# Performance work log

Hardware: AMD Instinct MI355X
Metric: run time of the kernel (lower is better)

## Reference

```python
import jax, jax.numpy as jnp
import numpy as np

N_SRC = 16384   # src nodes in block (includes dst nodes first, per DGL convention)
N_DST = 8192    # dst nodes
K = 32          # fixed in-degree per dst node -> dense mailbox [N_DST, K]
E = N_DST * K   # 262144 edges; edge i has dst node i // K
T = 16          # padded edge-sequence length
NODE_IN = 64
H = 64          # node_hidden_dim
E_IN = 8        # edge_in_dim
TH = 8          # time_hidden_dim
D_IN = E_IN + TH


def lstm_last(x, lengths, Wih, Whh, bih, bhh):
    """Unidirectional 1-layer LSTM; returns hidden state at step lengths-1 (pack_padded h_n).
    x: (E, T, D); lengths: (E,) in [1, T]. PyTorch gate order: i, f, g, o."""
    n, t_max, _ = x.shape
    h0 = jnp.zeros((n, H), x.dtype)

    def step(carry, xt):
        h, c, hlast, t = carry
        g = xt @ Wih.T + bih + h @ Whh.T + bhh
        i, f, gg, o = jnp.split(g, 4, axis=-1)
        c = jax.nn.sigmoid(f) * c + jax.nn.sigmoid(i) * jnp.tanh(gg)
        h = jax.nn.sigmoid(o) * jnp.tanh(c)
        hlast = jnp.where((t < lengths)[:, None], h, hlast)
        return (h, c, hlast, t + 1), None

    init = (h0, h0, h0, jnp.int32(0))
    (_, _, hlast, _), _ = jax.lax.scan(step, init, jnp.swapaxes(x, 0, 1))
    return hlast  # (E, H)


def sparsemax(z):
    """Sparsemax over last axis (Martins & Astudillo), matching the torch code."""
    z = z - jnp.max(z, axis=-1, keepdims=True)
    zs = -jnp.sort(-z, axis=-1)  # descending
    r = jnp.arange(1, z.shape[-1] + 1, dtype=z.dtype)
    bound = 1.0 + r * zs
    cs = jnp.cumsum(zs, axis=-1)
    is_gt = (bound > cs).astype(z.dtype)
    k = jnp.max(is_gt * r, axis=-1, keepdims=True)
    taus = (jnp.sum(is_gt * zs, axis=-1, keepdims=True) - 1.0) / k
    return jnp.maximum(z - taus, 0.0)


def setup_inputs():
    key = jax.random.key(0)
    ks = jax.random.split(key, 24)
    s = 0.1
    inp = {}
    inp["node_features"] = jax.random.normal(ks[0], (N_SRC, NODE_IN), jnp.float32)
    inp["edge_feats"] = jax.random.normal(ks[1], (E, T, E_IN), jnp.float32)
    inp["e_times"] = jax.random.uniform(ks[2], (E, T), jnp.float32)
    inp["e_len"] = jax.random.randint(ks[3], (E,), 1, T + 1).astype(jnp.int32)
    inp["edge_src"] = jax.random.randint(ks[4], (E,), 0, N_SRC).astype(jnp.int32)
    # Time2Vec (SineActivation) params: v = cat([sin(tau@w + b), tau@w0 + b0])
    inp["t2v_w"] = s * jax.random.normal(ks[5], (1, TH - 1), jnp.float32)
    inp["t2v_b"] = s * jax.random.normal(ks[6], (1, TH - 1), jnp.float32)
    inp["t2v_w0"] = s * jax.random.normal(ks[7], (1, 1), jnp.float32)
    inp["t2v_b0"] = s * jax.random.normal(ks[8], (1, 1), jnp.float32)
    # edge_layer LSTM
    inp["lstm_e_Wih"] = s * jax.random.normal(ks[9], (4 * H, D_IN), jnp.float32)
    inp["lstm_e_Whh"] = s * jax.random.normal(ks[10], (4 * H, H), jnp.float32)
    inp["lstm_e_bih"] = s * jax.random.normal(ks[11], (4 * H,), jnp.float32)
    inp["lstm_e_bhh"] = s * jax.random.normal(ks[12], (4 * H,), jnp.float32)
    # edge_attn_layer LSTM
    inp["lstm_a_Wih"] = s * jax.random.normal(ks[13], (4 * H, D_IN), jnp.float32)
    inp["lstm_a_Whh"] = s * jax.random.normal(ks[14], (4 * H, H), jnp.float32)
    inp["lstm_a_bih"] = s * jax.random.normal(ks[15], (4 * H,), jnp.float32)
    inp["lstm_a_bhh"] = s * jax.random.normal(ks[16], (4 * H,), jnp.float32)
    # attention scorer (no bias), edge_out and node linears
    inp["attn_w"] = s * jax.random.normal(ks[17], (H, 1), jnp.float32)
    inp["edge_out_W"] = s * jax.random.normal(ks[18], (H, NODE_IN + H), jnp.float32)
    inp["edge_out_b"] = s * jax.random.normal(ks[19], (H,), jnp.float32)
    inp["node_W"] = s * jax.random.normal(ks[20], (H, NODE_IN + H), jnp.float32)
    inp["node_b"] = s * jax.random.normal(ks[21], (H,), jnp.float32)
    return inp


def reference(node_features, edge_feats, e_times, t2v_w, t2v_b, t2v_w0, t2v_b0,
              lstm_e_Wih, lstm_e_Whh, lstm_e_bih, lstm_e_bhh,
              lstm_a_Wih, lstm_a_Whh, lstm_a_bih, lstm_a_bhh,
              attn_w, edge_out_W, edge_out_b, node_W, node_b,
              e_len, edge_src):
    h_src = node_features                 # dropout is identity in eval
    h_dst = node_features[:N_DST]
    # Time2Vec: tau (E, T, 1) -> (E, T, TH)
    tau = e_times[..., None]
    tenc = jnp.concatenate([jnp.sin(tau * t2v_w[0] + t2v_b[0]),
                            tau * t2v_w0[0] + t2v_b0[0]], axis=-1)
    e = jnp.concatenate([edge_feats, tenc], axis=-1)  # (E, T, D_IN)
    # per-edge LSTM encodings (last valid step)
    e_out = lstm_last(e, e_len, lstm_e_Wih, lstm_e_Whh, lstm_e_bih, lstm_e_bhh)  # (E, H)
    a_out = lstm_last(e, e_len, lstm_a_Wih, lstm_a_Whh, lstm_a_bih, lstm_a_bhh)  # (E, H)
    a = jax.nn.leaky_relu(a_out @ attn_w, 0.01)  # (E, 1)
    # per-edge message
    m = jax.nn.relu(jnp.concatenate([h_src[edge_src], e_out], axis=-1) @ edge_out_W.T + edge_out_b)  # (E, H)
    # reduce over ragged mailbox (regular degree K -> dense [N_DST, K, H])
    mb = m.reshape(N_DST, K, H)
    alpha = sparsemax(a.reshape(N_DST, K))[..., None]  # (N_DST, K, 1)
    h_neigh = jnp.sum(alpha * mb, axis=1)              # (N_DST, H)
    h = jax.nn.relu(jnp.concatenate([h_dst, h_neigh], axis=-1) @ node_W.T + node_b)
    return h  # (N_DST, H)
```

## Files before the change

kernel.cpp:

```cpp
#include <hip/hip_runtime.h>

typedef __bf16 bf16;
typedef __bf16 bf16x8 __attribute__((ext_vector_type(8)));
typedef float f32x4 __attribute__((ext_vector_type(4)));

#define N_DSTN 8192
#define TT 16
#define HROW 72
#define HBUF (32 * HROW)

#define WS_WHH  0
#define WS_WIH  65536
#define WS_BIAS 81920
#define WS_EW   83968
#define WS_NW   100352
#define WS_EB   116736
#define WS_NB   116992
#define WS_ATTN 117248
#define WS_T2W  117504
#define WS_T2B  117536

__device__ __forceinline__ f32x4 MFMA(bf16x8 a, bf16x8 b, f32x4 c) {
    return __builtin_amdgcn_mfma_f32_16x16x32_bf16(a, b, c, 0, 0, 0);
}
__device__ __forceinline__ float ldf(const void* p, long i, bool isb) {
    return isb ? (float)((const bf16*)p)[i] : ((const float*)p)[i];
}
__device__ __forceinline__ bf16x8 zero8() {
    bf16x8 z;
    #pragma unroll
    for (int i = 0; i < 8; i++) z[i] = (bf16)0.0f;
    return z;
}
__device__ __forceinline__ bf16x8 ld8v(const void* p, long i, bool isb) {
    if (isb) {
        return *reinterpret_cast<const bf16x8*>((const bf16*)p + i);
    } else {
        const float* f = (const float*)p + i;
        float4 u = *reinterpret_cast<const float4*>(f);
        float4 v = *reinterpret_cast<const float4*>(f + 4);
        bf16x8 r;
        r[0] = (bf16)u.x; r[1] = (bf16)u.y; r[2] = (bf16)u.z; r[3] = (bf16)u.w;
        r[4] = (bf16)v.x; r[5] = (bf16)v.y; r[6] = (bf16)v.z; r[7] = (bf16)v.w;
        return r;
    }
}

extern "C" __global__ void gtea_prep(const void* __restrict__ e_times,
                                     const void* __restrict__ t2v_w,
                                     const void* __restrict__ t2v_b,
                                     const void* __restrict__ t2v_w0,
                                     const void* __restrict__ t2v_b0,
                                     const void* __restrict__ Wih_e,
                                     const void* __restrict__ Whh_e,
                                     const void* __restrict__ bih_e,
                                     const void* __restrict__ bhh_e,
                                     const void* __restrict__ Wih_a,
                                     const void* __restrict__ Whh_a,
                                     const void* __restrict__ bih_a,
                                     const void* __restrict__ bhh_a,
                                     const void* __restrict__ attn_w,
                                     const void* __restrict__ edge_out_W,
                                     const void* __restrict__ edge_out_b,
                                     const void* __restrict__ node_W,
                                     const void* __restrict__ node_b,
                                     void* __restrict__ ws)
{
    __shared__ int isb_s;
    const int tid = threadIdx.x;
    if (tid < 64) {
        const unsigned short* u = (const unsigned short*)e_times;
        unsigned short a = u[tid * 2], b = u[tid * 2 + 1];
        bool ok = (a <= 0x3F80u) && (b <= 0x3F80u);
        unsigned long long m = __ballot(ok);
        if (tid == 0) isb_s = (m == ~0ULL) ? 1 : 0;
    }
    __syncthreads();
    const bool isb = (isb_s != 0);
    char* wsb = (char*)ws;
    const int gstep = blockDim.x * gridDim.x;
    const int g0 = blockIdx.x * blockDim.x + tid;

    for (int i = g0; i < 2 * 256 * 64; i += gstep) {
        int Lw = i >> 14, rem = i & 16383, n = rem >> 6;
        const void* W = Lw ? Whh_a : Whh_e;
        float gs = ((n >> 6) == 2) ? 2.88539008f : -1.44269504f;
        ((bf16*)(wsb + WS_WHH))[i] = (bf16)(ldf(W, rem, isb) * gs);
    }
    for (int i = g0; i < 2 * 256 * 16; i += gstep) {
        int Lw = i >> 12, rem = i & 4095, n = rem >> 4;
        const void* W = Lw ? Wih_a : Wih_e;
        float gs = ((n >> 6) == 2) ? 2.88539008f : -1.44269504f;
        ((bf16*)(wsb + WS_WIH))[i] = (bf16)(ldf(W, rem, isb) * gs);
    }
    for (int i = g0; i < 2 * 256; i += gstep) {
        int Lw = i >> 8, n = i & 255;
        const void* bi = Lw ? bih_a : bih_e;
        const void* bh = Lw ? bhh_a : bhh_e;
        float gs = ((n >> 6) == 2) ? 2.88539008f : -1.44269504f;
        ((float*)(wsb + WS_BIAS))[i] = (ldf(bi, n, isb) + ldf(bh, n, isb)) * gs;
    }
    for (int i = g0; i < 64 * 128; i += gstep) {
        ((bf16*)(wsb + WS_EW))[i] = (bf16)ldf(edge_out_W, i, isb);
        ((bf16*)(wsb + WS_NW))[i] = (bf16)ldf(node_W, i, isb);
    }
    for (int i = g0; i < 64; i += gstep) {
        ((float*)(wsb + WS_EB))[i]   = ldf(edge_out_b, i, isb);
        ((float*)(wsb + WS_NB))[i]   = ldf(node_b, i, isb);
        ((float*)(wsb + WS_ATTN))[i] = ldf(attn_w, i, isb);
    }
    if (g0 < 7) {
        ((float*)(wsb + WS_T2W))[g0] = ldf(t2v_w, g0, isb);
        ((float*)(wsb + WS_T2B))[g0] = ldf(t2v_b, g0, isb);
    }
    if (g0 == 7) {
        ((float*)(wsb + WS_T2W))[7] = ldf(t2v_w0, 0, isb);
        ((float*)(wsb + WS_T2B))[7] = ldf(t2v_b0, 0, isb);
    }
}

extern "C" __global__ void __launch_bounds__(512, 4)
gtea_fused(const void* __restrict__ node_features,
           const void* __restrict__ edge_feats,
           const void* __restrict__ e_times,
           const int*  __restrict__ e_len,
           const int*  __restrict__ edge_src,
           const void* __restrict__ ws,
           void* __restrict__ outp)
{
    __shared__ __align__(16) bf16 habuf[2][2][HBUF];
    __shared__ __align__(16) bf16 featb[TT * 32 * 8];
    __shared__ __align__(16) bf16 tb[TT * 32 * 8];
    __shared__ float t2w[8], t2b[8];
    __shared__ float attn_f[64];
    __shared__ float vbuf[128];
    __shared__ float scores_sh[32], alpha_sh[32];
    __shared__ int   lens_sh[32], idx_sh[32];
    __shared__ int   isb_sh;

    const int tid = threadIdx.x;
    const int w   = tid >> 6;
    const int l   = tid & 63;
    const int l15 = l & 15;
    const int q   = l >> 4;
    const int L   = w >> 2;
    const int w4  = w & 3;
    const int u16 = w4 * 16 + l15;

    const int d  = blockIdx.x;
    const int e0 = d * 32;
    const char* wsb = (const char*)ws;

    if (tid < 64) {
        const unsigned short* u = (const unsigned short*)e_times;
        unsigned short a = u[tid * 2], b = u[tid * 2 + 1];
        bool ok = (a <= 0x3F80u) && (b <= 0x3F80u);
        unsigned long long m = __ballot(ok);
        if (tid == 0) isb_sh = (m == ~0ULL) ? 1 : 0;
    }
    if (tid < 32) {
        int lj = e_len[e0 + tid];
        int rank = 0;
        for (int i = 0; i < 32; i++) {
            int li = __shfl(lj, i);
            rank += (li > lj) || (li == lj && i < tid);
        }
        int mt = rank >> 4, kp = rank & 15;
        int slot = mt * 16 + (kp & 3) * 4 + (kp >> 2);
        idx_sh[slot]  = tid;
        lens_sh[slot] = lj;
    }
    __syncthreads();
    const bool isb = (isb_sh != 0);

    if (tid < 8)  { t2w[tid] = ((const float*)(wsb + WS_T2W))[tid];
                    t2b[tid] = ((const float*)(wsb + WS_T2B))[tid]; }
    if (tid < 64) attn_f[tid] = ((const float*)(wsb + WS_ATTN))[tid];
    if (tid < 64) vbuf[tid] = ldf(node_features, (long)d * 64 + tid, isb);
    {
        unsigned int* hz = reinterpret_cast<unsigned int*>(&habuf[0][0][0]);
        for (int i = tid; i < HBUF / 2; i += 512) { hz[i] = 0u; hz[i + HBUF] = 0u; }
    }
    __syncthreads();

    int gm0[4], gm1[4];
    #pragma unroll
    for (int r = 0; r < 4; r++) {
        gm0[r] = __builtin_amdgcn_readfirstlane(lens_sh[r]);
        gm1[r] = __builtin_amdgcn_readfirstlane(lens_sh[16 + r]);
    }
    const int tmax = gm0[0], mtmax1 = gm1[0];

    unsigned lp = 0;
    #pragma unroll
    for (int mt = 0; mt < 2; mt++)
        #pragma unroll
        for (int r = 0; r < 4; r++)
            lp |= (unsigned)(lens_sh[mt * 16 + q * 4 + r] - 1) << ((mt * 4 + r) * 4);

    {
        int s = tid >> 4, t = tid & 15;
        int j = idx_sh[s];
        long base = ((long)(e0 + j) * TT + t) * 8;
        *reinterpret_cast<bf16x8*>(&featb[(t * 32 + s) * 8]) = ld8v(edge_feats, base, isb);
        float tau = ldf(e_times, (long)(e0 + j) * TT + t, isb);
        bf16x8 te;
        #pragma unroll
        for (int i = 0; i < 7; i++) te[i] = (bf16)__sinf(tau * t2w[i] + t2b[i]);
        te[7] = (bf16)(tau * t2w[7] + t2b[7]);
        *reinterpret_cast<bf16x8*>(&tb[(t * 32 + s) * 8]) = te;
    }

    const bf16*  wWhh  = (const bf16*)(wsb + WS_WHH) + (long)L * 256 * 64;
    const bf16*  wWih  = (const bf16*)(wsb + WS_WIH) + (long)L * 256 * 16;
    const float* wBias = (const float*)(wsb + WS_BIAS) + L * 256;
    bf16x8 Bh[4][2], Bx[4];
    float  bias[4];
    #pragma unroll
    for (int j = 0; j < 4; j++) {
        int n = 64 * j + u16;
        Bh[j][0] = *reinterpret_cast<const bf16x8*>(wWhh + (long)n * 64 + q * 8);
        Bh[j][1] = *reinterpret_cast<const bf16x8*>(wWhh + (long)n * 64 + 32 + q * 8);
        Bx[j] = (q < 2) ? *reinterpret_cast<const bf16x8*>(wWih + (long)n * 16 + q * 8) : zero8();
        bias[j] = wBias[n];
    }

    float c[2][4];
    #pragma unroll
    for (int mt = 0; mt < 2; mt++)
        #pragma unroll
        for (int r = 0; r < 4; r++) c[mt][r] = 0.0f;

    __syncthreads();

    bf16* hb_base = &habuf[L][0][0];
    const int rd_off = l15 * HROW + q * 8;
    const int wr_off = (q * 4) * HROW + u16;

    for (int t = 0; t < tmax; t++) {
        const bf16* hbR = hb_base + (t & 1) * HBUF;
        bf16*       hbW = hb_base + ((t + 1) & 1) * HBUF;

        auto do_mt = [&](int mt) {
            const bf16* hr = hbR + mt * (16 * HROW) + rd_off;
            bf16x8 ah0 = *reinterpret_cast<const bf16x8*>(hr);
            bf16x8 ah1 = *reinterpret_cast<const bf16x8*>(hr + 32);
            bf16x8 xa;
            if (q < 2) {
                const bf16* xp = (q == 0 ? featb : tb) + (t * 32 + mt * 16 + l15) * 8;
                xa = *reinterpret_cast<const bf16x8*>(xp);
            } else {
                xa = zero8();
            }
            f32x4 D[4];
            #pragma unroll
            for (int j = 0; j < 4; j++) {
                f32x4 acc = {bias[j], bias[j], bias[j], bias[j]};
                acc = MFMA(ah0, Bh[j][0], acc);
                acc = MFMA(ah1, Bh[j][1], acc);
                acc = MFMA(xa,  Bx[j],    acc);
                D[j] = acc;
            }
            bf16* hw = hbW + mt * (16 * HROW) + wr_off;
            #pragma unroll
            for (int r = 0; r < 4; r++) {
                int gmax = mt ? gm1[r] : gm0[r];
                if (t < gmax) {
                    int lm1 = (int)((lp >> ((mt * 4 + r) * 4)) & 15u);
                    if (t <= lm1) {
                        float gi = D[0][r], gf = D[1][r];
                        float gg = D[2][r], go = D[3][r];
                        float ei = __builtin_amdgcn_exp2f(gi);
                        float ef = __builtin_amdgcn_exp2f(gf);
                        float eg = __builtin_amdgcn_exp2f(gg);
                        float di = 1.0f + ei, dfv = 1.0f + ef, dg = 1.0f + eg;
                        float m1 = di * dg;
                        float R1 = __builtin_amdgcn_rcpf(m1 * dfv);
                        float cn = (m1 * R1) * c[mt][r] + (eg - 1.0f) * (dfv * R1);
                        c[mt][r] = cn;
                        float eo = __builtin_amdgcn_exp2f(go);
                        float ec = __builtin_amdgcn_exp2f(2.88539008f * cn);
                        float R2 = __builtin_amdgcn_rcpf((1.0f + eo) * (1.0f + ec));
                        float hn = (ec - 1.0f) * R2;
                        hw[r * HROW] = (bf16)hn;
                    }
                }
            }
        };
        do_mt(0);
        if (t < mtmax1) do_mt(1);
        __syncthreads();
    }

    if (tid < 256) {
        int s = tid >> 3, c8 = tid & 7;
        const bf16* ha = &habuf[1][lens_sh[s] & 1][s * HROW];
        float p = 0.0f;
        #pragma unroll
        for (int i = 0; i < 8; i++)
            p += (float)ha[c8 * 8 + i] * attn_f[c8 * 8 + i];
        p += __shfl_xor(p, 1);
        p += __shfl_xor(p, 2);
        p += __shfl_xor(p, 4);
        if (c8 == 0) scores_sh[s] = (p > 0.0f) ? p : 0.01f * p;
    }
    float mval[2][4];
    if (tid < 256) {
        const bf16* wEW = (const bf16*)(wsb + WS_EW);
        bf16x8 Bw[4];
        #pragma unroll
        for (int ks = 0; ks < 4; ks++)
            Bw[ks] = *reinterpret_cast<const bf16x8*>(wEW + (long)u16 * 128 + ks * 32 + q * 8);
        float mb = ((const float*)(wsb + WS_EB))[u16];
        #pragma unroll
        for (int mt = 0; mt < 2; mt++) {
            int s = mt * 16 + l15;
            int src = edge_src[e0 + idx_sh[s]];
            bf16x8 a0 = ld8v(node_features, (long)src * 64 + q * 8, isb);
            bf16x8 a1 = ld8v(node_features, (long)src * 64 + 32 + q * 8, isb);
            const bf16* he = &habuf[0][lens_sh[s] & 1][s * HROW];
            bf16x8 a2 = *reinterpret_cast<const bf16x8*>(he + q * 8);
            bf16x8 a3 = *reinterpret_cast<const bf16x8*>(he + 32 + q * 8);
            f32x4 acc = {mb, mb, mb, mb};
            acc = MFMA(a0, Bw[0], acc);
            acc = MFMA(a1, Bw[1], acc);
            acc = MFMA(a2, Bw[2], acc);
            acc = MFMA(a3, Bw[3], acc);
            #pragma unroll
            for (int r = 0; r < 4; r++) mval[mt][r] = fmaxf(acc[r], 0.0f);
        }
    }
    __syncthreads();

    if (tid < 64) {
        float z = (tid < 32) ? scores_sh[tid] : -3.0e38f;
        float zm = z;
        #pragma unroll
        for (int m = 32; m >= 1; m >>= 1) zm = fmaxf(zm, __shfl_xor(zm, m));
        z -= zm;
        int cnt = 0; float sb = 0.0f;
        for (int i = 0; i < 32; i++) {
            float zi = __shfl(z, i);
            bool before = (zi > z) || (zi == z && i < tid);
            if (before) { cnt++; sb += zi; }
        }
        float r = (float)(cnt + 1);
        float S = sb + z;
        bool isgt = (tid < 32) && (1.0f + r * z > S);
        float kf  = isgt ? r : 0.0f;
        float sgt = isgt ? z : 0.0f;
        #pragma unroll
        for (int m = 32; m >= 1; m >>= 1) kf = fmaxf(kf, __shfl_xor(kf, m));
        #pragma unroll
        for (int m = 32; m >= 1; m >>= 1) sgt += __shfl_xor(sgt, m);
        float tau = (sgt - 1.0f) / fmaxf(kf, 1.0f);
        if (tid < 32) alpha_sh[tid] = fmaxf(z - tau, 0.0f);
    }
    __syncthreads();

    if (tid < 256) {
        float hn = 0.0f;
        #pragma unroll
        for (int mt = 0; mt < 2; mt++)
            #pragma unroll
            for (int r = 0; r < 4; r++)
                hn += alpha_sh[mt * 16 + q * 4 + r] * mval[mt][r];
        hn += __shfl_xor(hn, 16);
        hn += __shfl_xor(hn, 32);
        if (q == 0) vbuf[64 + u16] = hn;
    }
    __syncthreads();

    if (tid < 256) {
        int u = tid >> 2, kq = tid & 3;
        const bf16* wNW = (const bf16*)(wsb + WS_NW);
        bf16x8 wv0 = *reinterpret_cast<const bf16x8*>(wNW + (long)u * 128 + kq * 32);
        bf16x8 wv1 = *reinterpret_cast<const bf16x8*>(wNW + (long)u * 128 + kq * 32 + 8);
        bf16x8 wv2 = *reinterpret_cast<const bf16x8*>(wNW + (long)u * 128 + kq * 32 + 16);
        bf16x8 wv3 = *reinterpret_cast<const bf16x8*>(wNW + (long)u * 128 + kq * 32 + 24);
        float acc = 0.0f;
        #pragma unroll
        for (int i = 0; i < 8; i++) {
            acc += (float)wv0[i] * vbuf[kq * 32 + i];
            acc += (float)wv1[i] * vbuf[kq * 32 + 8 + i];
            acc += (float)wv2[i] * vbuf[kq * 32 + 16 + i];
            acc += (float)wv3[i] * vbuf[kq * 32 + 24 + i];
        }
        acc += __shfl_xor(acc, 1);
        acc += __shfl_xor(acc, 2);
        if (kq == 0) {
            float s = acc + ((const float*)(wsb + WS_NB))[u];
            float v = fmaxf(s, 0.0f);
            long o = (long)d * 64 + u;
            if (isb) ((bf16*)outp)[o] = (bf16)v;
            else     ((float*)outp)[o] = v;
        }
    }
}

extern "C" void kernel_launch(void* const* d_in, const int* in_sizes, int n_in,
                              void* d_out, int out_size, void* d_ws, size_t ws_size,
                              hipStream_t stream) {
    gtea_prep<<<32, 256, 0, stream>>>(
        d_in[2],
        d_in[5], d_in[6], d_in[7], d_in[8],
        d_in[9], d_in[10], d_in[11], d_in[12],
        d_in[13], d_in[14], d_in[15], d_in[16],
        d_in[17], d_in[18], d_in[19],
        d_in[20], d_in[21],
        d_ws);
    gtea_fused<<<N_DSTN, 512, 0, stream>>>(
        d_in[0], d_in[1], d_in[2],
        (const int*)d_in[3], (const int*)d_in[4],
        d_ws, d_out);
}
```

Baseline: 714.5 us.

## Move Wih fragments to LDS, interleave x buffers, and raise occupancy bound

Raises the launch-bounds minimum blocks from 4 to 6 to push for higher occupancy. To free registers it drops the per-thread Wih B-fragments and instead stages Wih in shared memory, reading it inside the recurrent loop. A zero row stands in for the masked lanes. The edge-feature and time-encoding buffers are merged into one interleaved buffer, and the ping-pong h-buffer pointers are swapped instead of recomputed each step. This trades extra LDS reads on the serial LSTM critical path, plus extra LDS per block, for fewer VGPRs and more resident waves.

```diff
diff --git a/kernel.cpp b/kernel.cpp
--- a/kernel.cpp
+++ b/kernel.cpp
@@ -25,12 +25,6 @@
 }
 __device__ __forceinline__ float ldf(const void* p, long i, bool isb) {
     return isb ? (float)((const bf16*)p)[i] : ((const float*)p)[i];
-}
-__device__ __forceinline__ bf16x8 zero8() {
-    bf16x8 z;
-    #pragma unroll
-    for (int i = 0; i < 8; i++) z[i] = (bf16)0.0f;
-    return z;
 }
 __device__ __forceinline__ bf16x8 ld8v(const void* p, long i, bool isb) {
     if (isb) {
@@ -119,7 +113,7 @@
     }
 }
 
-extern "C" __global__ void __launch_bounds__(512, 4)
+extern "C" __global__ void __launch_bounds__(512, 6)
 gtea_fused(const void* __restrict__ node_features,
            const void* __restrict__ edge_feats,
            const void* __restrict__ e_times,
@@ -129,8 +123,8 @@
            void* __restrict__ outp)
 {
     __shared__ __align__(16) bf16 habuf[2][2][HBUF];
-    __shared__ __align__(16) bf16 featb[TT * 32 * 8];
-    __shared__ __align__(16) bf16 tb[TT * 32 * 8];
+    __shared__ __align__(16) bf16 xb[TT * 32 * 16];
+    __shared__ __align__(16) bf16 wihb[2 * 256 * 16 + 16];
     __shared__ float t2w[8], t2b[8];
     __shared__ float attn_f[64];
     __shared__ float vbuf[128];
@@ -181,6 +175,13 @@
         unsigned int* hz = reinterpret_cast<unsigned int*>(&habuf[0][0][0]);
         for (int i = tid; i < HBUF / 2; i += 512) { hz[i] = 0u; hz[i + HBUF] = 0u; }
     }
+    {
+        #pragma unroll
+        for (int i = 0; i < 2; i++)
+            reinterpret_cast<bf16x8*>(wihb)[tid + i * 512] =
+                reinterpret_cast<const bf16x8*>(wsb + WS_WIH)[tid + i * 512];
+        if (tid < 16) wihb[2 * 256 * 16 + tid] = (bf16)0.0f;
+    }
     __syncthreads();
 
     int gm0[4], gm1[4];
@@ -202,28 +203,33 @@
         int s = tid >> 4, t = tid & 15;
         int j = idx_sh[s];
         long base = ((long)(e0 + j) * TT + t) * 8;
-        *reinterpret_cast<bf16x8*>(&featb[(t * 32 + s) * 8]) = ld8v(edge_feats, base, isb);
+        *reinterpret_cast<bf16x8*>(&xb[(t * 32 + s) * 16]) = ld8v(edge_feats, base, isb);
         float tau = ldf(e_times, (long)(e0 + j) * TT + t, isb);
         bf16x8 te;
         #pragma unroll
         for (int i = 0; i < 7; i++) te[i] = (bf16)__sinf(tau * t2w[i] + t2b[i]);
         te[7] = (bf16)(tau * t2w[7] + t2b[7]);
-        *reinterpret_cast<bf16x8*>(&tb[(t * 32 + s) * 8]) = te;
+        *reinterpret_cast<bf16x8*>(&xb[(t * 32 + s) * 16 + 8]) = te;
     }
 
     const bf16*  wWhh  = (const bf16*)(wsb + WS_WHH) + (long)L * 256 * 64;
-    const bf16*  wWih  = (const bf16*)(wsb + WS_WIH) + (long)L * 256 * 16;
     const float* wBias = (const float*)(wsb + WS_BIAS) + L * 256;
-    bf16x8 Bh[4][2], Bx[4];
+    bf16x8 Bh[4][2];
     float  bias[4];
     #pragma unroll
     for (int j = 0; j < 4; j++) {
         int n = 64 * j + u16;
         Bh[j][0] = *reinterpret_cast<const bf16x8*>(wWhh + (long)n * 64 + q * 8);
         Bh[j][1] = *reinterpret_cast<const bf16x8*>(wWhh + (long)n * 64 + 32 + q * 8);
-        Bx[j] = (q < 2) ? *reinterpret_cast<const bf16x8*>(wWih + (long)n * 16 + q * 8) : zero8();
         bias[j] = wBias[n];
     }
+
+    const bf16* zrow = &wihb[2 * 256 * 16];
+    const bf16* bxp  = (q < 2) ? &wihb[(L * 256 + u16) * 16 + q * 8] : zrow;
+    const int   bx_str = (q < 2) ? (64 * 16) : 0;
+    const bf16* xpt  = (q < 2) ? &xb[l15 * 16 + q * 8] : zrow;
+    const int   xa_t = (q < 2) ? (32 * 16) : 0;
+    const int   xa_m = (q < 2) ? (16 * 16) : 0;
 
     float c[2][4];
     #pragma unroll
@@ -236,32 +242,28 @@
     bf16* hb_base = &habuf[L][0][0];
     const int rd_off = l15 * HROW + q * 8;
     const int wr_off = (q * 4) * HROW + u16;
+    const bf16* rp = hb_base + rd_off;
+    bf16*       wp = hb_base + HBUF + wr_off;
+    const bf16* rpo = hb_base + HBUF + rd_off;
+    bf16*       wpo = hb_base + wr_off;
 
     for (int t = 0; t < tmax; t++) {
-        const bf16* hbR = hb_base + (t & 1) * HBUF;
-        bf16*       hbW = hb_base + ((t + 1) & 1) * HBUF;
-
         auto do_mt = [&](int mt) {
-            const bf16* hr = hbR + mt * (16 * HROW) + rd_off;
+            const bf16* hr = rp + mt * (16 * HROW);
             bf16x8 ah0 = *reinterpret_cast<const bf16x8*>(hr);
             bf16x8 ah1 = *reinterpret_cast<const bf16x8*>(hr + 32);
-            bf16x8 xa;
-            if (q < 2) {
-                const bf16* xp = (q == 0 ? featb : tb) + (t * 32 + mt * 16 + l15) * 8;
-                xa = *reinterpret_cast<const bf16x8*>(xp);
-            } else {
-                xa = zero8();
-            }
+            bf16x8 xa  = *reinterpret_cast<const bf16x8*>(xpt + mt * xa_m);
             f32x4 D[4];
             #pragma unroll
             for (int j = 0; j < 4; j++) {
                 f32x4 acc = {bias[j], bias[j], bias[j], bias[j]};
                 acc = MFMA(ah0, Bh[j][0], acc);
                 acc = MFMA(ah1, Bh[j][1], acc);
-                acc = MFMA(xa,  Bx[j],    acc);
+                bf16x8 bx = *reinterpret_cast<const bf16x8*>(bxp + j * bx_str);
+                acc = MFMA(xa, bx, acc);
                 D[j] = acc;
             }
-            bf16* hw = hbW + mt * (16 * HROW) + wr_off;
+            bf16* hw = wp + mt * (16 * HROW);
             #pragma unroll
             for (int r = 0; r < 4; r++) {
                 int gmax = mt ? gm1[r] : gm0[r];
@@ -289,6 +291,9 @@
         };
         do_mt(0);
         if (t < mtmax1) do_mt(1);
+        const bf16* tr = rp; rp = rpo; rpo = tr;
+        bf16* tw = wp; wp = wpo; wpo = tw;
+        xpt += xa_t;
         __syncthreads();
     }
 
```

After: 1.629 ms. 2.28x slower.
